# Optimization experiments

Measured on AMD Instinct MI355X. Metric: run time of the kernel, lower is better.

The kernel has to match this reference:

```python
import jax, jax.numpy as jnp
import numpy as np

C_IN = 32
H = W = 256          # LR feature map
HQ = WQ = 256        # query grid
NC = 3               # output channels
LAT = C_IN * 9 + 2 + 2  # 292


def setup_inputs() -> dict:
    key = jax.random.key(0)
    ks = jax.random.split(key, 12)
    features = jax.random.normal(ks[0], (1, C_IN, H, W), jnp.float32)
    locations = jax.random.uniform(ks[1], (HQ, WQ, 2), jnp.float32, -1.0, 1.0)
    cell_sizes = jnp.full((HQ, WQ, 2), 2.0 / HQ, jnp.float32)
    dims = [LAT, 256, 256, 256, 256, NC]
    inp = {"features": features, "locations": locations, "cell_sizes": cell_sizes}
    for i in range(5):
        fin, fout = dims[i], dims[i + 1]
        inp[f"w{i+1}"] = jax.random.normal(ks[2 + i], (fin, fout), jnp.float32) * (1.0 / np.sqrt(fin))
        inp[f"b{i+1}"] = jnp.zeros((fout,), jnp.float32)
    return inp


def _liif_forward(features, locations, cell_sizes, ws, bs):
    B, C, h, w = features.shape
    # reflect-pad + 3x3 unfold -> [B, C*9, h, w] (torch unfold order: c slow, (ki,kj) fast)
    pad = jnp.pad(features, ((0, 0), (0, 0), (1, 1), (1, 1)), mode="reflect")
    patches = jnp.stack([pad[:, :, i:i + h, j:j + w] for i in range(3) for j in range(3)], axis=2)
    feat = patches.reshape(B, C * 9, h, w)[0]  # only batch 0 is used by the module

    rx, ry, eps = 1.0 / h, 1.0 / w, 1e-6
    shifts = jnp.array([[-1., -1.], [-1., 1.], [1., -1.], [1., 1.]], jnp.float32)  # (vx,vy) order
    loc = locations[None] + shifts[:, None, None, :] * jnp.array([rx, ry], jnp.float32) + eps
    loc = jnp.clip(loc, -1.0 + 1e-6, 1.0 - 1e-6)  # [4,HQ,WQ,2]

    # nearest grid_sample, align_corners=False: unnormalize then round
    iy = jnp.clip(jnp.round(((loc[..., 0] + 1.0) * h - 1.0) * 0.5).astype(jnp.int32), 0, h - 1)
    ix = jnp.clip(jnp.round(((loc[..., 1] + 1.0) * w - 1.0) * 0.5).astype(jnp.int32), 0, w - 1)

    q_feat = feat[:, iy, ix].transpose(1, 2, 3, 0)  # [4,HQ,WQ,C*9]
    # feat_coord gather == pixel-center coordinate of nearest cell
    qy = -1.0 + (2.0 * iy + 1.0) / h
    qx = -1.0 + (2.0 * ix + 1.0) / w
    rel = jnp.stack([(locations[..., 0][None] - qy) * h,
                     (locations[..., 1][None] - qx) * w], axis=-1)  # [4,HQ,WQ,2]

    rel_cell = cell_sizes * jnp.array([h, w], jnp.float32)
    rel_cell = jnp.broadcast_to(rel_cell[None], (4,) + rel_cell.shape)

    x = jnp.concatenate([q_feat, rel, rel_cell], axis=-1)  # [4,HQ,WQ,292]
    for wl, bl in zip(ws[:-1], bs[:-1]):
        x = jax.nn.relu(x @ wl + bl)
    pred = x @ ws[-1] + bs[-1]  # [4,HQ,WQ,NC]

    area = jnp.abs(rel[..., 0] * rel[..., 1]) + 1e-9  # [4,HQ,WQ]
    tot = area.sum(axis=0)
    area_sw = area[::-1]  # swap 0<->3, 1<->2 as in the module
    return (pred * (area_sw / tot)[..., None]).sum(axis=0)  # [HQ,WQ,NC]


def reference(features, locations, cell_sizes, w1, b1, w2, b2, w3, b3, w4, b4, w5, b5):
    return _liif_forward(features, locations, cell_sizes,
                         [w1, w2, w3, w4, w5], [b1, b2, b3, b4, b5])
```

## Files before the change

### kernel.cpp

```cpp
#include <hip/hip_runtime.h>

typedef _Float16 half8 __attribute__((ext_vector_type(8)));
typedef _Float16 half4 __attribute__((ext_vector_type(4)));
typedef float f32x4 __attribute__((ext_vector_type(4)));

#define SA 320
#define MROW 128

__global__ void liif_prep(const float* __restrict__ feat,
                          const float* __restrict__ w1, const float* __restrict__ w2,
                          const float* __restrict__ w3, const float* __restrict__ w4,
                          const float* __restrict__ w5,
                          _Float16* __restrict__ featT,
                          _Float16* __restrict__ wt1, _Float16* __restrict__ wt2,
                          _Float16* __restrict__ wt3, _Float16* __restrict__ wt4,
                          _Float16* __restrict__ wt5) {
  const int blk = blockIdx.x, tid = threadIdx.x;
  if (blk < 256) {
    const int px = blk * 256 + tid;
    _Float16 v[32];
#pragma unroll
    for (int c = 0; c < 32; ++c) v[c] = (_Float16)feat[(c << 16) + px];
    half8* dst = (half8*)(featT + px * 32);
#pragma unroll
    for (int j = 0; j < 4; ++j) dst[j] = *(half8*)(v + j * 8);
    return;
  }
  int i = (blk - 256) * 256 + tid;
  if (i < 81920) {
    const int n = i / 320, kcol = i % 320;
    float v = 0.f;
    if (kcol < 288) {
      const int k = kcol >> 5, c = kcol & 31;
      v = w1[(c * 9 + k) * 256 + n];
    } else if (kcol < 292) {
      v = w1[kcol * 256 + n];
    }
    wt1[i] = (_Float16)v;
    return;
  }
  i -= 81920;
  if (i < 196608) {
    const int li = i >> 16, r = i & 65535;
    const int n = r >> 8, k = r & 255;
    const float* w = (li == 0) ? w2 : ((li == 1) ? w3 : w4);
    _Float16* wt = (li == 0) ? wt2 : ((li == 1) ? wt3 : wt4);
    wt[r] = (_Float16)w[k * 256 + n];
    return;
  }
  i -= 196608;
  if (i < 4096) {
    const int n = i >> 8, k = i & 255;
    wt5[i] = (n < 3) ? (_Float16)w5[k * 3 + n] : (_Float16)0.f;
  }
}

__device__ __forceinline__ void row_params(int r, const float* __restrict__ loc,
                                           const float* __restrict__ cell,
                                           int& iy, int& ix, float& rel0v, float& rel1v,
                                           float& c0v, float& c1v) {
  const int q = r >> 2, s = r & 3;
  const float loc0 = loc[q * 2 + 0], loc1 = loc[q * 2 + 1];
  const float shy = (s & 2) ? 1.f : -1.f;
  const float shx = (s & 1) ? 1.f : -1.f;
  const float rxy = 1.f / 256.f;
  float l0 = __fadd_rn(loc0 + shy * rxy, 1e-6f);
  float l1 = __fadd_rn(loc1 + shx * rxy, 1e-6f);
  const float lo = -1.f + 1e-6f, hi = 1.f - 1e-6f;
  l0 = fminf(fmaxf(l0, lo), hi);
  l1 = fminf(fmaxf(l1, lo), hi);
  iy = (int)rintf(__fmul_rn(__fadd_rn(__fmul_rn(__fadd_rn(l0, 1.f), 256.f), -1.f), 0.5f));
  ix = (int)rintf(__fmul_rn(__fadd_rn(__fmul_rn(__fadd_rn(l1, 1.f), 256.f), -1.f), 0.5f));
  iy = min(max(iy, 0), 255);
  ix = min(max(ix, 0), 255);
  const float qy = -1.f + (float)(2 * iy + 1) * (1.f / 256.f);
  const float qx = -1.f + (float)(2 * ix + 1) * (1.f / 256.f);
  rel0v = __fmul_rn(__fsub_rn(loc0, qy), 256.f);
  rel1v = __fmul_rn(__fsub_rn(loc1, qx), 256.f);
  c0v = cell[q * 2 + 0] * 256.f;
  c1v = cell[q * 2 + 1] * 256.f;
}

template <int NSTEPS, int KW>
__device__ __forceinline__ void layer_mm(const _Float16* __restrict__ wt,
                                         f32x4 acc[4][8],
                                         const _Float16* sA, int w, int lane) {
  const int ln = lane & 15, qd = lane >> 4, e = ln & 7;
  const _Float16* ab[4];
  const _Float16* bb[8];
#pragma unroll
  for (int mt = 0; mt < 4; ++mt)
    ab[mt] = wt + (w * 64 + mt * 16 + ln) * KW + qd * 8;
#pragma unroll
  for (int nt = 0; nt < 8; ++nt)
    bb[nt] = sA + (nt * 16 + ln) * SA;
#pragma unroll
  for (int st = 0; st < NSTEPS; ++st) {
    const int off = ((((st << 2) | qd) ^ e) << 3);
    half8 a[4], b[8];
#pragma unroll
    for (int mt = 0; mt < 4; ++mt) a[mt] = *(const half8*)(ab[mt] + st * 32);
#pragma unroll
    for (int nt = 0; nt < 8; ++nt) b[nt] = *(const half8*)(bb[nt] + off);
#pragma unroll
    for (int mt = 0; mt < 4; ++mt)
#pragma unroll
      for (int nt = 0; nt < 8; ++nt)
        acc[mt][nt] =
            __builtin_amdgcn_mfma_f32_16x16x32_f16(a[mt], b[nt], acc[mt][nt], 0, 0, 0);
  }
}

__device__ __forceinline__ void epilogue_relu(f32x4 acc[4][8], _Float16* sA,
                                              const float* __restrict__ bias,
                                              int w, int lane) {
  __syncthreads();
  const int ln = lane & 15, q4 = (lane >> 4) << 2;
#pragma unroll
  for (int mt = 0; mt < 4; ++mt) {
    const int f = w * 64 + mt * 16 + q4;
    const f32x4 bv = *(const f32x4*)(bias + f);
    const int chunk = f >> 3;
#pragma unroll
    for (int nt = 0; nt < 8; ++nt) {
      const int row = nt * 16 + ln;
      half4 h;
#pragma unroll
      for (int r = 0; r < 4; ++r) {
        h[r] = (_Float16)fmaxf(acc[mt][nt][r] + bv[r], 0.f);
        acc[mt][nt][r] = 0.f;
      }
      const int pos = chunk ^ (row & 7);
      *(half4*)(sA + row * SA + pos * 8 + (f & 7)) = h;
    }
  }
  __syncthreads();
}

__global__ __launch_bounds__(256, 2) void liif_main(
    const _Float16* __restrict__ featT,
    const float* __restrict__ loc, const float* __restrict__ cell,
    const float* __restrict__ b1, const float* __restrict__ b2,
    const float* __restrict__ b3, const float* __restrict__ b4,
    const float* __restrict__ b5,
    const _Float16* __restrict__ wt1, const _Float16* __restrict__ wt2,
    const _Float16* __restrict__ wt3, const _Float16* __restrict__ wt4,
    const _Float16* __restrict__ wt5,
    float* __restrict__ out) {
  extern __shared__ __align__(16) _Float16 sAct[];

  const int tid = threadIdx.x;
  const int w = tid >> 6, lane = tid & 63;
  const int blk = blockIdx.x;

  {
    const int row = tid >> 1, part = tid & 1;
    int iy, ix; float rel0v, rel1v, c0v, c1v;
    row_params(blk * MROW + row, loc, cell, iy, ix, rel0v, rel1v, c0v, c1v);
    const int y0 = (iy == 0) ? 1 : iy - 1;
    const int y2 = (iy == 255) ? 254 : iy + 1;
    const int x0 = (ix == 0) ? 1 : ix - 1;
    const int x2 = (ix == 255) ? 254 : ix + 1;
    _Float16* arow = sAct + row * SA;
    const int eor = row & 7;
#pragma unroll
    for (int k = 0; k < 9; ++k) {
      const int dy = k / 3, dx = k % 3;
      const int y = (dy == 0) ? y0 : ((dy == 1) ? iy : y2);
      const int x = (dx == 0) ? x0 : ((dx == 1) ? ix : x2);
      const half8* src = (const half8*)(featT + ((y << 8) + x) * 32 + part * 16);
#pragma unroll
      for (int j = 0; j < 2; ++j) {
        const int pos = (k * 4 + part * 2 + j) ^ eor;
        *(half8*)(arow + pos * 8) = src[j];
      }
    }
#pragma unroll
    for (int j = 0; j < 2; ++j) {
      half8 tv = {};
      if (part == 0 && j == 0) {
        tv[0] = (_Float16)rel0v;
        tv[1] = (_Float16)rel1v;
        tv[2] = (_Float16)c0v;
        tv[3] = (_Float16)c1v;
      }
      const int pos = (36 + part * 2 + j) ^ eor;
      *(half8*)(arow + pos * 8) = tv;
    }
  }

  f32x4 acc[4][8];
#pragma unroll
  for (int mt = 0; mt < 4; ++mt)
#pragma unroll
    for (int nt = 0; nt < 8; ++nt)
      acc[mt][nt] = (f32x4){0.f, 0.f, 0.f, 0.f};

  __syncthreads();

  layer_mm<10, 320>(wt1, acc, sAct, w, lane);
  epilogue_relu(acc, sAct, b1, w, lane);
  layer_mm<8, 256>(wt2, acc, sAct, w, lane);
  epilogue_relu(acc, sAct, b2, w, lane);
  layer_mm<8, 256>(wt3, acc, sAct, w, lane);
  epilogue_relu(acc, sAct, b3, w, lane);
  layer_mm<8, 256>(wt4, acc, sAct, w, lane);
  epilogue_relu(acc, sAct, b4, w, lane);

  {
    const int ln = lane & 15, qd = lane >> 4, e = ln & 7;
#pragma unroll
    for (int nt = 0; nt < 2; ++nt) {
      f32x4 a5 = {0.f, 0.f, 0.f, 0.f};
      const _Float16* abp = wt5 + ln * 256 + qd * 8;
      const _Float16* bbp = sAct + (w * 32 + nt * 16 + ln) * SA;
#pragma unroll
      for (int st = 0; st < 8; ++st) {
        const int off = ((((st << 2) | qd) ^ e) << 3);
        const half8 a = *(const half8*)(abp + st * 32);
        const half8 b = *(const half8*)(bbp + off);
        a5 = __builtin_amdgcn_mfma_f32_16x16x32_f16(a, b, a5, 0, 0, 0);
      }
      int iy, ix; float rel0v, rel1v, c0v, c1v;
      row_params(blk * MROW + w * 32 + nt * 16 + ln, loc, cell,
                 iy, ix, rel0v, rel1v, c0v, c1v);
      const float area = fabsf(rel0v * rel1v) + 1e-9f;
      float t = area + __shfl_xor(area, 1);
      const float tot = t + __shfl_xor(t, 2);
      const float asw = __shfl_xor(area, 3);
      const float wr = asw / tot;
      float v0 = (a5[0] + b5[0]) * wr;
      float v1 = (a5[1] + b5[1]) * wr;
      float v2 = (a5[2] + b5[2]) * wr;
      v0 += __shfl_xor(v0, 1); v0 += __shfl_xor(v0, 2);
      v1 += __shfl_xor(v1, 1); v1 += __shfl_xor(v1, 2);
      v2 += __shfl_xor(v2, 1); v2 += __shfl_xor(v2, 2);
      if (qd == 0 && (ln & 3) == 0) {
        const int q = blk * 32 + w * 8 + nt * 4 + (ln >> 2);
        out[q * 3 + 0] = v0;
        out[q * 3 + 1] = v1;
        out[q * 3 + 2] = v2;
      }
    }
  }
}

extern "C" void kernel_launch(void* const* d_in, const int* in_sizes, int n_in,
                              void* d_out, int out_size, void* d_ws, size_t ws_size,
                              hipStream_t stream) {
  (void)in_sizes; (void)n_in; (void)out_size; (void)ws_size;
  const float* feat = (const float*)d_in[0];
  const float* loc  = (const float*)d_in[1];
  const float* cell = (const float*)d_in[2];
  const float* w1 = (const float*)d_in[3];  const float* b1 = (const float*)d_in[4];
  const float* w2 = (const float*)d_in[5];  const float* b2 = (const float*)d_in[6];
  const float* w3 = (const float*)d_in[7];  const float* b3 = (const float*)d_in[8];
  const float* w4 = (const float*)d_in[9];  const float* b4 = (const float*)d_in[10];
  const float* w5 = (const float*)d_in[11]; const float* b5 = (const float*)d_in[12];

  char* ws = (char*)d_ws;
  _Float16* featT = (_Float16*)(ws);
  _Float16* wt1 = (_Float16*)(ws + 4194304);
  _Float16* wt2 = (_Float16*)(ws + 4358144);
  _Float16* wt3 = (_Float16*)(ws + 4489216);
  _Float16* wt4 = (_Float16*)(ws + 4620288);
  _Float16* wt5 = (_Float16*)(ws + 4751360);

  liif_prep<<<1360, 256, 0, stream>>>(feat, w1, w2, w3, w4, w5,
                                      featT, wt1, wt2, wt3, wt4, wt5);
  liif_main<<<2048, 256, MROW * SA * 2, stream>>>(featT, loc, cell,
                                                  b1, b2, b3, b4, b5,
                                                  wt1, wt2, wt3, wt4, wt5,
                                                  (float*)d_out);
}
```

Baseline: 246.1 us.

## Switch MLP layers to 32x32x16 MFMA tiles with weight prefetch

```diff
diff --git a/kernel.cpp b/kernel.cpp
--- a/kernel.cpp
+++ b/kernel.cpp
@@ -3,6 +3,7 @@
 typedef _Float16 half8 __attribute__((ext_vector_type(8)));
 typedef _Float16 half4 __attribute__((ext_vector_type(4)));
 typedef float f32x4 __attribute__((ext_vector_type(4)));
+typedef float f32x16 __attribute__((ext_vector_type(16)));
 
 #define SA 320
 #define MROW 128
@@ -28,30 +29,26 @@
   }
   int i = (blk - 256) * 256 + tid;
   if (i < 81920) {
-    const int n = i / 320, kcol = i % 320;
+    const int n = i & 255, col = i >> 8;
     float v = 0.f;
-    if (kcol < 288) {
-      const int k = kcol >> 5, c = kcol & 31;
-      v = w1[(c * 9 + k) * 256 + n];
-    } else if (kcol < 292) {
-      v = w1[kcol * 256 + n];
-    }
-    wt1[i] = (_Float16)v;
+    if (col < 288) v = w1[((col & 31) * 9 + (col >> 5)) * 256 + n];
+    else if (col < 292) v = w1[col * 256 + n];
+    wt1[n * 320 + col] = (_Float16)v;
     return;
   }
   i -= 81920;
   if (i < 196608) {
     const int li = i >> 16, r = i & 65535;
-    const int n = r >> 8, k = r & 255;
+    const int k = r >> 8, n = r & 255;
     const float* w = (li == 0) ? w2 : ((li == 1) ? w3 : w4);
     _Float16* wt = (li == 0) ? wt2 : ((li == 1) ? wt3 : wt4);
-    wt[r] = (_Float16)w[k * 256 + n];
+    wt[n * 256 + k] = (_Float16)w[k * 256 + n];
     return;
   }
   i -= 196608;
   if (i < 4096) {
-    const int n = i >> 8, k = i & 255;
-    wt5[i] = (n < 3) ? (_Float16)w5[k * 3 + n] : (_Float16)0.f;
+    const int f = i >> 8, k = i & 255;
+    wt5[f * 256 + k] = (f < 3) ? (_Float16)w5[k * 3 + f] : (_Float16)0.f;
   }
 }
 
@@ -81,57 +78,71 @@
   c1v = cell[q * 2 + 1] * 256.f;
 }
 
+template <int KW>
+__device__ __forceinline__ void prefA(const _Float16* __restrict__ wt,
+                                      int w, int lane, half8* pa) {
+  const int m = lane & 31, qd = lane >> 5;
+  const _Float16* base = wt + (w * 64 + m) * KW + qd * 8;
+  pa[0] = *(const half8*)(base);
+  pa[1] = *(const half8*)(base + 32 * KW);
+}
+
 template <int NSTEPS, int KW>
-__device__ __forceinline__ void layer_mm(const _Float16* __restrict__ wt,
-                                         f32x4 acc[4][8],
-                                         const _Float16* sA, int w, int lane) {
-  const int ln = lane & 15, qd = lane >> 4, e = ln & 7;
-  const _Float16* ab[4];
-  const _Float16* bb[8];
-#pragma unroll
-  for (int mt = 0; mt < 4; ++mt)
-    ab[mt] = wt + (w * 64 + mt * 16 + ln) * KW + qd * 8;
-#pragma unroll
-  for (int nt = 0; nt < 8; ++nt)
-    bb[nt] = sA + (nt * 16 + ln) * SA;
+__device__ __forceinline__ void layer_mm32(const _Float16* __restrict__ wt,
+                                           f32x16 acc[2][4],
+                                           const _Float16* sA, int w, int lane,
+                                           const half8* pa) {
+  const int m = lane & 31, qd = lane >> 5, e = lane & 7;
+  const _Float16* ab0 = wt + (w * 64 + m) * KW + qd * 8;
+  const _Float16* bb[4];
+#pragma unroll
+  for (int rt = 0; rt < 4; ++rt) bb[rt] = sA + (rt * 32 + m) * SA;
 #pragma unroll
   for (int st = 0; st < NSTEPS; ++st) {
-    const int off = ((((st << 2) | qd) ^ e) << 3);
-    half8 a[4], b[8];
-#pragma unroll
-    for (int mt = 0; mt < 4; ++mt) a[mt] = *(const half8*)(ab[mt] + st * 32);
-#pragma unroll
-    for (int nt = 0; nt < 8; ++nt) b[nt] = *(const half8*)(bb[nt] + off);
-#pragma unroll
-    for (int mt = 0; mt < 4; ++mt)
-#pragma unroll
-      for (int nt = 0; nt < 8; ++nt)
-        acc[mt][nt] =
-            __builtin_amdgcn_mfma_f32_16x16x32_f16(a[mt], b[nt], acc[mt][nt], 0, 0, 0);
-  }
-}
-
-__device__ __forceinline__ void epilogue_relu(f32x4 acc[4][8], _Float16* sA,
-                                              const float* __restrict__ bias,
-                                              int w, int lane) {
+    const int off = ((st * 2 + qd) ^ e) * 8;
+    half8 a[2], b[4];
+    if (st == 0) {
+      a[0] = pa[0]; a[1] = pa[1];
+    } else {
+      a[0] = *(const half8*)(ab0 + st * 16);
+      a[1] = *(const half8*)(ab0 + 32 * KW + st * 16);
+    }
+#pragma unroll
+    for (int rt = 0; rt < 4; ++rt) b[rt] = *(const half8*)(bb[rt] + off);
+#pragma unroll
+    for (int ft = 0; ft < 2; ++ft)
+#pragma unroll
+      for (int rt = 0; rt < 4; ++rt)
+        acc[ft][rt] = __builtin_amdgcn_mfma_f32_32x32x16_f16(a[ft], b[rt],
+                                                             acc[ft][rt], 0, 0, 0);
+  }
+}
+
+__device__ __forceinline__ void epilogue32(f32x16 acc[2][4], _Float16* sA,
+                                           const float* __restrict__ bias,
+                                           int w, int lane) {
   __syncthreads();
-  const int ln = lane & 15, q4 = (lane >> 4) << 2;
-#pragma unroll
-  for (int mt = 0; mt < 4; ++mt) {
-    const int f = w * 64 + mt * 16 + q4;
-    const f32x4 bv = *(const f32x4*)(bias + f);
-    const int chunk = f >> 3;
-#pragma unroll
-    for (int nt = 0; nt < 8; ++nt) {
-      const int row = nt * 16 + ln;
-      half4 h;
-#pragma unroll
-      for (int r = 0; r < 4; ++r) {
-        h[r] = (_Float16)fmaxf(acc[mt][nt][r] + bv[r], 0.f);
-        acc[mt][nt][r] = 0.f;
-      }
-      const int pos = chunk ^ (row & 7);
-      *(half4*)(sA + row * SA + pos * 8 + (f & 7)) = h;
+  const int n = lane & 31, qd = lane >> 5;
+#pragma unroll
+  for (int ft = 0; ft < 2; ++ft) {
+    const int fbase = w * 64 + ft * 32;
+#pragma unroll
+    for (int g = 0; g < 4; ++g) {
+      const int f0 = fbase + g * 8 + qd * 4;
+      const f32x4 bv = *(const f32x4*)(bias + f0);
+      const int chunk = (fbase >> 3) + g;
+#pragma unroll
+      for (int rt = 0; rt < 4; ++rt) {
+        const int row = rt * 32 + n;
+        half4 h;
+#pragma unroll
+        for (int r = 0; r < 4; ++r) {
+          h[r] = (_Float16)fmaxf(acc[ft][rt][g * 4 + r] + bv[r], 0.f);
+          acc[ft][rt][g * 4 + r] = 0.f;
+        }
+        const int pos = chunk ^ (row & 7);
+        *(half4*)(sA + row * SA + pos * 8 + qd * 4) = h;
+      }
     }
   }
   __syncthreads();
@@ -153,6 +164,9 @@
   const int w = tid >> 6, lane = tid & 63;
   const int blk = blockIdx.x;
 
+  half8 pa[2];
+  prefA<320>(wt1, w, lane, pa);
+
   {
     const int row = tid >> 1, part = tid & 1;
     int iy, ix; float rel0v, rel1v, c0v, c1v;
@@ -189,23 +203,27 @@
     }
   }
 
-  f32x4 acc[4][8];
-#pragma unroll
-  for (int mt = 0; mt < 4; ++mt)
-#pragma unroll
-    for (int nt = 0; nt < 8; ++nt)
-      acc[mt][nt] = (f32x4){0.f, 0.f, 0.f, 0.f};
+  f32x16 acc[2][4];
+#pragma unroll
+  for (int ft = 0; ft < 2; ++ft)
+#pragma unroll
+    for (int rt = 0; rt < 4; ++rt)
+#pragma unroll
+      for (int r = 0; r < 16; ++r) acc[ft][rt][r] = 0.f;
 
   __syncthreads();
 
-  layer_mm<10, 320>(wt1, acc, sAct, w, lane);
-  epilogue_relu(acc, sAct, b1, w, lane);
-  layer_mm<8, 256>(wt2, acc, sAct, w, lane);
-  epilogue_relu(acc, sAct, b2, w, lane);
-  layer_mm<8, 256>(wt3, acc, sAct, w, lane);
-  epilogue_relu(acc, sAct, b3, w, lane);
-  layer_mm<8, 256>(wt4, acc, sAct, w, lane);
-  epilogue_relu(acc, sAct, b4, w, lane);
+  layer_mm32<20, 320>(wt1, acc, sAct, w, lane, pa);
+  prefA<256>(wt2, w, lane, pa);
+  epilogue32(acc, sAct, b1, w, lane);
+  layer_mm32<16, 256>(wt2, acc, sAct, w, lane, pa);
+  prefA<256>(wt3, w, lane, pa);
+  epilogue32(acc, sAct, b2, w, lane);
+  layer_mm32<16, 256>(wt3, acc, sAct, w, lane, pa);
+  prefA<256>(wt4, w, lane, pa);
+  epilogue32(acc, sAct, b3, w, lane);
+  layer_mm32<16, 256>(wt4, acc, sAct, w, lane, pa);
+  epilogue32(acc, sAct, b4, w, lane);
 
   {
     const int ln = lane & 15, qd = lane >> 4, e = ln & 7;
```

Result: slower. 265.9 us (+8.1%).

## Re-tile MLP warps 2x2 and double-buffer weight and activation fragment loads

Applied to the files above, without the earlier changes.

```diff
diff --git a/kernel.cpp b/kernel.cpp
--- a/kernel.cpp
+++ b/kernel.cpp
@@ -28,30 +28,26 @@
   }
   int i = (blk - 256) * 256 + tid;
   if (i < 81920) {
-    const int n = i / 320, kcol = i % 320;
+    const int n = i & 255, col = i >> 8;
     float v = 0.f;
-    if (kcol < 288) {
-      const int k = kcol >> 5, c = kcol & 31;
-      v = w1[(c * 9 + k) * 256 + n];
-    } else if (kcol < 292) {
-      v = w1[kcol * 256 + n];
-    }
-    wt1[i] = (_Float16)v;
+    if (col < 288) v = w1[((col & 31) * 9 + (col >> 5)) * 256 + n];
+    else if (col < 292) v = w1[col * 256 + n];
+    wt1[n * 320 + col] = (_Float16)v;
     return;
   }
   i -= 81920;
   if (i < 196608) {
     const int li = i >> 16, r = i & 65535;
-    const int n = r >> 8, k = r & 255;
+    const int k = r >> 8, n = r & 255;
     const float* w = (li == 0) ? w2 : ((li == 1) ? w3 : w4);
     _Float16* wt = (li == 0) ? wt2 : ((li == 1) ? wt3 : wt4);
-    wt[r] = (_Float16)w[k * 256 + n];
+    wt[n * 256 + k] = (_Float16)w[k * 256 + n];
     return;
   }
   i -= 196608;
   if (i < 4096) {
-    const int n = i >> 8, k = i & 255;
-    wt5[i] = (n < 3) ? (_Float16)w5[k * 3 + n] : (_Float16)0.f;
+    const int f = i >> 8, k = i & 255;
+    wt5[f * 256 + k] = (f < 3) ? (_Float16)w5[k * 3 + f] : (_Float16)0.f;
   }
 }
 
@@ -81,49 +77,69 @@
   c1v = cell[q * 2 + 1] * 256.f;
 }
 
+template <int KW>
+__device__ __forceinline__ void prefA(const _Float16* __restrict__ wt,
+                                      int fh, int lane, half8* pa) {
+  const int ln = lane & 15, qd = lane >> 4;
+#pragma unroll
+  for (int mt = 0; mt < 8; ++mt)
+    pa[mt] = *(const half8*)(wt + (fh + mt * 16 + ln) * KW + qd * 8);
+}
+
 template <int NSTEPS, int KW>
 __device__ __forceinline__ void layer_mm(const _Float16* __restrict__ wt,
-                                         f32x4 acc[4][8],
-                                         const _Float16* sA, int w, int lane) {
+                                         f32x4 acc[8][4],
+                                         const _Float16* sA, int fh, int rh,
+                                         int lane, const half8* pa) {
   const int ln = lane & 15, qd = lane >> 4, e = ln & 7;
-  const _Float16* ab[4];
-  const _Float16* bb[8];
-#pragma unroll
-  for (int mt = 0; mt < 4; ++mt)
-    ab[mt] = wt + (w * 64 + mt * 16 + ln) * KW + qd * 8;
-#pragma unroll
-  for (int nt = 0; nt < 8; ++nt)
-    bb[nt] = sA + (nt * 16 + ln) * SA;
+  const _Float16* ab[8];
+#pragma unroll
+  for (int mt = 0; mt < 8; ++mt)
+    ab[mt] = wt + (fh + mt * 16 + ln) * KW + qd * 8;
+  const _Float16* bb[4];
+#pragma unroll
+  for (int nt = 0; nt < 4; ++nt)
+    bb[nt] = sA + (rh + nt * 16 + ln) * SA;
+  half8 a[2][8], b[2][4];
+#pragma unroll
+  for (int mt = 0; mt < 8; ++mt) a[0][mt] = pa[mt];
+#pragma unroll
+  for (int nt = 0; nt < 4; ++nt)
+    b[0][nt] = *(const half8*)(bb[nt] + ((qd ^ e) << 3));
 #pragma unroll
   for (int st = 0; st < NSTEPS; ++st) {
-    const int off = ((((st << 2) | qd) ^ e) << 3);
-    half8 a[4], b[8];
-#pragma unroll
-    for (int mt = 0; mt < 4; ++mt) a[mt] = *(const half8*)(ab[mt] + st * 32);
-#pragma unroll
-    for (int nt = 0; nt < 8; ++nt) b[nt] = *(const half8*)(bb[nt] + off);
-#pragma unroll
-    for (int mt = 0; mt < 4; ++mt)
-#pragma unroll
-      for (int nt = 0; nt < 8; ++nt)
-        acc[mt][nt] =
-            __builtin_amdgcn_mfma_f32_16x16x32_f16(a[mt], b[nt], acc[mt][nt], 0, 0, 0);
-  }
-}
-
-__device__ __forceinline__ void epilogue_relu(f32x4 acc[4][8], _Float16* sA,
+    const int cur = st & 1, nxt = cur ^ 1;
+    if (st + 1 < NSTEPS) {
+#pragma unroll
+      for (int mt = 0; mt < 8; ++mt)
+        a[nxt][mt] = *(const half8*)(ab[mt] + (st + 1) * 32);
+      const int off = ((((st + 1) << 2) | qd) ^ e) << 3;
+#pragma unroll
+      for (int nt = 0; nt < 4; ++nt)
+        b[nxt][nt] = *(const half8*)(bb[nt] + off);
+    }
+#pragma unroll
+    for (int mt = 0; mt < 8; ++mt)
+#pragma unroll
+      for (int nt = 0; nt < 4; ++nt)
+        acc[mt][nt] = __builtin_amdgcn_mfma_f32_16x16x32_f16(a[cur][mt], b[cur][nt],
+                                                             acc[mt][nt], 0, 0, 0);
+  }
+}
+
+__device__ __forceinline__ void epilogue_relu(f32x4 acc[8][4], _Float16* sA,
                                               const float* __restrict__ bias,
-                                              int w, int lane) {
+                                              int fh, int rh, int lane) {
   __syncthreads();
   const int ln = lane & 15, q4 = (lane >> 4) << 2;
 #pragma unroll
-  for (int mt = 0; mt < 4; ++mt) {
-    const int f = w * 64 + mt * 16 + q4;
+  for (int mt = 0; mt < 8; ++mt) {
+    const int f = fh + mt * 16 + q4;
     const f32x4 bv = *(const f32x4*)(bias + f);
     const int chunk = f >> 3;
 #pragma unroll
-    for (int nt = 0; nt < 8; ++nt) {
-      const int row = nt * 16 + ln;
+    for (int nt = 0; nt < 4; ++nt) {
+      const int row = rh + nt * 16 + ln;
       half4 h;
 #pragma unroll
       for (int r = 0; r < 4; ++r) {
@@ -151,7 +167,11 @@
 
   const int tid = threadIdx.x;
   const int w = tid >> 6, lane = tid & 63;
+  const int fh = (w & 1) * 128, rh = (w >> 1) * 64;
   const int blk = blockIdx.x;
+
+  half8 pa[8];
+  prefA<320>(wt1, fh, lane, pa);
 
   {
     const int row = tid >> 1, part = tid & 1;
@@ -189,23 +209,26 @@
     }
   }
 
-  f32x4 acc[4][8];
-#pragma unroll
-  for (int mt = 0; mt < 4; ++mt)
-#pragma unroll
-    for (int nt = 0; nt < 8; ++nt)
+  f32x4 acc[8][4];
+#pragma unroll
+  for (int mt = 0; mt < 8; ++mt)
+#pragma unroll
+    for (int nt = 0; nt < 4; ++nt)
       acc[mt][nt] = (f32x4){0.f, 0.f, 0.f, 0.f};
 
   __syncthreads();
 
-  layer_mm<10, 320>(wt1, acc, sAct, w, lane);
-  epilogue_relu(acc, sAct, b1, w, lane);
-  layer_mm<8, 256>(wt2, acc, sAct, w, lane);
-  epilogue_relu(acc, sAct, b2, w, lane);
-  layer_mm<8, 256>(wt3, acc, sAct, w, lane);
-  epilogue_relu(acc, sAct, b3, w, lane);
-  layer_mm<8, 256>(wt4, acc, sAct, w, lane);
-  epilogue_relu(acc, sAct, b4, w, lane);
+  layer_mm<10, 320>(wt1, acc, sAct, fh, rh, lane, pa);
+  prefA<256>(wt2, fh, lane, pa);
+  epilogue_relu(acc, sAct, b1, fh, rh, lane);
+  layer_mm<8, 256>(wt2, acc, sAct, fh, rh, lane, pa);
+  prefA<256>(wt3, fh, lane, pa);
+  epilogue_relu(acc, sAct, b2, fh, rh, lane);
+  layer_mm<8, 256>(wt3, acc, sAct, fh, rh, lane, pa);
+  prefA<256>(wt4, fh, lane, pa);
+  epilogue_relu(acc, sAct, b3, fh, rh, lane);
+  layer_mm<8, 256>(wt4, acc, sAct, fh, rh, lane, pa);
+  epilogue_relu(acc, sAct, b4, fh, rh, lane);
 
   {
     const int ln = lane & 15, qd = lane >> 4, e = ln & 7;
```

Measured after the change: 360.9 us. 1.47x slower.

## Shrink row tile to 80 rows for three blocks per CU occupancy

Applied to the files above, without the earlier changes.

```diff
diff --git a/kernel.cpp b/kernel.cpp
--- a/kernel.cpp
+++ b/kernel.cpp
@@ -5,7 +5,7 @@
 typedef float f32x4 __attribute__((ext_vector_type(4)));
 
 #define SA 320
-#define MROW 128
+#define MROW 80
 
 __global__ void liif_prep(const float* __restrict__ feat,
                           const float* __restrict__ w1, const float* __restrict__ w2,
@@ -28,30 +28,26 @@
   }
   int i = (blk - 256) * 256 + tid;
   if (i < 81920) {
-    const int n = i / 320, kcol = i % 320;
+    const int n = i & 255, col = i >> 8;
     float v = 0.f;
-    if (kcol < 288) {
-      const int k = kcol >> 5, c = kcol & 31;
-      v = w1[(c * 9 + k) * 256 + n];
-    } else if (kcol < 292) {
-      v = w1[kcol * 256 + n];
-    }
-    wt1[i] = (_Float16)v;
+    if (col < 288) v = w1[((col & 31) * 9 + (col >> 5)) * 256 + n];
+    else if (col < 292) v = w1[col * 256 + n];
+    wt1[n * 320 + col] = (_Float16)v;
     return;
   }
   i -= 81920;
   if (i < 196608) {
     const int li = i >> 16, r = i & 65535;
-    const int n = r >> 8, k = r & 255;
+    const int k = r >> 8, n = r & 255;
     const float* w = (li == 0) ? w2 : ((li == 1) ? w3 : w4);
     _Float16* wt = (li == 0) ? wt2 : ((li == 1) ? wt3 : wt4);
-    wt[r] = (_Float16)w[k * 256 + n];
+    wt[n * 256 + k] = (_Float16)w[k * 256 + n];
     return;
   }
   i -= 196608;
   if (i < 4096) {
-    const int n = i >> 8, k = i & 255;
-    wt5[i] = (n < 3) ? (_Float16)w5[k * 3 + n] : (_Float16)0.f;
+    const int f = i >> 8, k = i & 255;
+    wt5[f * 256 + k] = (f < 3) ? (_Float16)w5[k * 3 + f] : (_Float16)0.f;
   }
 }
 
@@ -83,46 +79,44 @@
 
 template <int NSTEPS, int KW>
 __device__ __forceinline__ void layer_mm(const _Float16* __restrict__ wt,
-                                         f32x4 acc[4][8],
-                                         const _Float16* sA, int w, int lane) {
+                                         f32x4 acc[4][5],
+                                         const _Float16* sA, int fh, int lane) {
   const int ln = lane & 15, qd = lane >> 4, e = ln & 7;
   const _Float16* ab[4];
-  const _Float16* bb[8];
 #pragma unroll
   for (int mt = 0; mt < 4; ++mt)
-    ab[mt] = wt + (w * 64 + mt * 16 + ln) * KW + qd * 8;
-#pragma unroll
-  for (int nt = 0; nt < 8; ++nt)
-    bb[nt] = sA + (nt * 16 + ln) * SA;
+    ab[mt] = wt + (fh + mt * 16 + ln) * KW + qd * 8;
+  const _Float16* bbase = sA + ln * SA;
 #pragma unroll
   for (int st = 0; st < NSTEPS; ++st) {
     const int off = ((((st << 2) | qd) ^ e) << 3);
-    half8 a[4], b[8];
+    half8 a[4], b[5];
 #pragma unroll
     for (int mt = 0; mt < 4; ++mt) a[mt] = *(const half8*)(ab[mt] + st * 32);
 #pragma unroll
-    for (int nt = 0; nt < 8; ++nt) b[nt] = *(const half8*)(bb[nt] + off);
+    for (int nt = 0; nt < 5; ++nt)
+      b[nt] = *(const half8*)(bbase + nt * 16 * SA + off);
 #pragma unroll
     for (int mt = 0; mt < 4; ++mt)
 #pragma unroll
-      for (int nt = 0; nt < 8; ++nt)
-        acc[mt][nt] =
-            __builtin_amdgcn_mfma_f32_16x16x32_f16(a[mt], b[nt], acc[mt][nt], 0, 0, 0);
-  }
-}
-
-__device__ __forceinline__ void epilogue_relu(f32x4 acc[4][8], _Float16* sA,
+      for (int nt = 0; nt < 5; ++nt)
+        acc[mt][nt] = __builtin_amdgcn_mfma_f32_16x16x32_f16(a[mt], b[nt],
+                                                             acc[mt][nt], 0, 0, 0);
+  }
+}
+
+__device__ __forceinline__ void epilogue_relu(f32x4 acc[4][5], _Float16* sA,
                                               const float* __restrict__ bias,
-                                              int w, int lane) {
+                                              int fh, int lane) {
   __syncthreads();
   const int ln = lane & 15, q4 = (lane >> 4) << 2;
 #pragma unroll
   for (int mt = 0; mt < 4; ++mt) {
-    const int f = w * 64 + mt * 16 + q4;
+    const int f = fh + mt * 16 + q4;
     const f32x4 bv = *(const f32x4*)(bias + f);
     const int chunk = f >> 3;
 #pragma unroll
-    for (int nt = 0; nt < 8; ++nt) {
+    for (int nt = 0; nt < 5; ++nt) {
       const int row = nt * 16 + ln;
       half4 h;
 #pragma unroll
@@ -137,7 +131,7 @@
   __syncthreads();
 }
 
-__global__ __launch_bounds__(256, 2) void liif_main(
+__global__ __launch_bounds__(256, 3) void liif_main(
     const _Float16* __restrict__ featT,
     const float* __restrict__ loc, const float* __restrict__ cell,
     const float* __restrict__ b1, const float* __restrict__ b2,
@@ -151,69 +145,71 @@
 
   const int tid = threadIdx.x;
   const int w = tid >> 6, lane = tid & 63;
+  const int fh = w * 64;
   const int blk = blockIdx.x;
 
-  {
-    const int row = tid >> 1, part = tid & 1;
+  for (int it = tid; it < MROW * 10; it += 256) {
+    const int row = it / 10, tap = it - row * 10;
+    int rg = blk * MROW + row;
+    rg = min(rg, 262143);
     int iy, ix; float rel0v, rel1v, c0v, c1v;
-    row_params(blk * MROW + row, loc, cell, iy, ix, rel0v, rel1v, c0v, c1v);
-    const int y0 = (iy == 0) ? 1 : iy - 1;
-    const int y2 = (iy == 255) ? 254 : iy + 1;
-    const int x0 = (ix == 0) ? 1 : ix - 1;
-    const int x2 = (ix == 255) ? 254 : ix + 1;
+    row_params(rg, loc, cell, iy, ix, rel0v, rel1v, c0v, c1v);
     _Float16* arow = sAct + row * SA;
     const int eor = row & 7;
-#pragma unroll
-    for (int k = 0; k < 9; ++k) {
-      const int dy = k / 3, dx = k % 3;
+    if (tap < 9) {
+      const int dy = tap / 3, dx = tap % 3;
+      const int y0 = (iy == 0) ? 1 : iy - 1;
+      const int y2 = (iy == 255) ? 254 : iy + 1;
+      const int x0 = (ix == 0) ? 1 : ix - 1;
+      const int x2 = (ix == 255) ? 254 : ix + 1;
       const int y = (dy == 0) ? y0 : ((dy == 1) ? iy : y2);
       const int x = (dx == 0) ? x0 : ((dx == 1) ? ix : x2);
-      const half8* src = (const half8*)(featT + ((y << 8) + x) * 32 + part * 16);
-#pragma unroll
-      for (int j = 0; j < 2; ++j) {
-        const int pos = (k * 4 + part * 2 + j) ^ eor;
+      const half8* src = (const half8*)(featT + ((y << 8) + x) * 32);
+#pragma unroll
+      for (int j = 0; j < 4; ++j) {
+        const int pos = (tap * 4 + j) ^ eor;
         *(half8*)(arow + pos * 8) = src[j];
       }
+    } else {
+#pragma unroll
+      for (int j = 0; j < 4; ++j) {
+        half8 tv = {};
+        if (j == 0) {
+          tv[0] = (_Float16)rel0v;
+          tv[1] = (_Float16)rel1v;
+          tv[2] = (_Float16)c0v;
+          tv[3] = (_Float16)c1v;
+        }
+        const int pos = (36 + j) ^ eor;
+        *(half8*)(arow + pos * 8) = tv;
+      }
     }
-#pragma unroll
-    for (int j = 0; j < 2; ++j) {
-      half8 tv = {};
-      if (part == 0 && j == 0) {
-        tv[0] = (_Float16)rel0v;
-        tv[1] = (_Float16)rel1v;
-        tv[2] = (_Float16)c0v;
-        tv[3] = (_Float16)c1v;
-      }
-      const int pos = (36 + part * 2 + j) ^ eor;
-      *(half8*)(arow + pos * 8) = tv;
-    }
-  }
-
-  f32x4 acc[4][8];
+  }
+
+  f32x4 acc[4][5];
 #pragma unroll
   for (int mt = 0; mt < 4; ++mt)
 #pragma unroll
-    for (int nt = 0; nt < 8; ++nt)
+    for (int nt = 0; nt < 5; ++nt)
       acc[mt][nt] = (f32x4){0.f, 0.f, 0.f, 0.f};
 
   __syncthreads();
 
-  layer_mm<10, 320>(wt1, acc, sAct, w, lane);
-  epilogue_relu(acc, sAct, b1, w, lane);
-  layer_mm<8, 256>(wt2, acc, sAct, w, lane);
-  epilogue_relu(acc, sAct, b2, w, lane);
-  layer_mm<8, 256>(wt3, acc, sAct, w, lane);
-  epilogue_relu(acc, sAct, b3, w, lane);
-  layer_mm<8, 256>(wt4, acc, sAct, w, lane);
-  epilogue_relu(acc, sAct, b4, w, lane);
+  layer_mm<10, 320>(wt1, acc, sAct, fh, lane);
+  epilogue_relu(acc, sAct, b1, fh, lane);
+  layer_mm<8, 256>(wt2, acc, sAct, fh, lane);
+  epilogue_relu(acc, sAct, b2, fh, lane);
+  layer_mm<8, 256>(wt3, acc, sAct, fh, lane);
+  epilogue_relu(acc, sAct, b3, fh, lane);
+  layer_mm<8, 256>(wt4, acc, sAct, fh, lane);
+  epilogue_relu(acc, sAct, b4, fh, lane);
 
   {
     const int ln = lane & 15, qd = lane >> 4, e = ln & 7;
-#pragma unroll
-    for (int nt = 0; nt < 2; ++nt) {
+    for (int t = w; t < 5; t += 4) {
       f32x4 a5 = {0.f, 0.f, 0.f, 0.f};
       const _Float16* abp = wt5 + ln * 256 + qd * 8;
-      const _Float16* bbp = sAct + (w * 32 + nt * 16 + ln) * SA;
+      const _Float16* bbp = sAct + (t * 16 + ln) * SA;
 #pragma unroll
       for (int st = 0; st < 8; ++st) {
         const int off = ((((st << 2) | qd) ^ e) << 3);
@@ -221,12 +217,14 @@
         const half8 b = *(const half8*)(bbp + off);
         a5 = __builtin_amdgcn_mfma_f32_16x16x32_f16(a, b, a5, 0, 0, 0);
       }
+      int rg = blk * MROW + t * 16 + ln;
+      const bool valid = rg < 262144;
+      rg = min(rg, 262143);
       int iy, ix; float rel0v, rel1v, c0v, c1v;
-      row_params(blk * MROW + w * 32 + nt * 16 + ln, loc, cell,
-                 iy, ix, rel0v, rel1v, c0v, c1v);
+      row_params(rg, loc, cell, iy, ix, rel0v, rel1v, c0v, c1v);
       const float area = fabsf(rel0v * rel1v) + 1e-9f;
-      float t = area + __shfl_xor(area, 1);
-      const float tot = t + __shfl_xor(t, 2);
+      float tsum = area + __shfl_xor(area, 1);
+      const float tot = tsum + __shfl_xor(tsum, 2);
       const float asw = __shfl_xor(area, 3);
       const float wr = asw / tot;
       float v0 = (a5[0] + b5[0]) * wr;
@@ -235,8 +233,8 @@
       v0 += __shfl_xor(v0, 1); v0 += __shfl_xor(v0, 2);
       v1 += __shfl_xor(v1, 1); v1 += __shfl_xor(v1, 2);
       v2 += __shfl_xor(v2, 1); v2 += __shfl_xor(v2, 2);
-      if (qd == 0 && (ln & 3) == 0) {
-        const int q = blk * 32 + w * 8 + nt * 4 + (ln >> 2);
+      if (qd == 0 && (ln & 3) == 0 && valid) {
+        const int q = blk * 20 + t * 4 + (ln >> 2);
         out[q * 3 + 0] = v0;
         out[q * 3 + 1] = v1;
         out[q * 3 + 2] = v2;
@@ -268,7 +266,7 @@
 
   liif_prep<<<1360, 256, 0, stream>>>(feat, w1, w2, w3, w4, w5,
                                       featT, wt1, wt2, wt3, wt4, wt5);
-  liif_main<<<2048, 256, MROW * SA * 2, stream>>>(featT, loc, cell,
+  liif_main<<<3277, 256, MROW * SA * 2, stream>>>(featT, loc, cell,
                                                   b1, b2, b3, b4, b5,
                                                   wt1, wt2, wt3, wt4, wt5,
                                                   (float*)d_out);
```

Result: slower. 350.6 us (+42.5%).
